# Kernel tuning notes

Hardware: AMD Instinct MI355X
Metric: run time of the kernel (lower is better)

## Reference

```python
import jax, jax.numpy as jnp
import numpy as np

B, NR, NP, E, F, EIN, H, OUT = 2, 16384, 65536, 262144, 128, 4, 16, 4
EPS = 1e-6

def _mlp(x, W1, b1, W2, b2):
    return jax.nn.swish(x @ W1 + b1) @ W2 + b2

def _cond_norm(x, tau, C1, c1, C2, c2):
    # conditioned LayerNorm: scale/shift computed from tau by a shallow MLP
    h = jax.nn.swish(tau @ C1 + c1)               # [B, H]
    scale, shift = jnp.split(h @ C2 + c2, 2, -1)  # [B, F] each
    mu = jnp.mean(x, -1, keepdims=True)
    var = jnp.var(x, -1, keepdims=True)
    xn = (x - mu) * jax.lax.rsqrt(var + EPS)
    return xn * (1.0 + scale[:, None, :]) + shift[:, None, :]

def _segment_mean(feat, recv, num_segments):
    seg = lambda f, r: jax.ops.segment_sum(f, r, num_segments=num_segments)
    s = jax.vmap(seg)(feat, recv)
    cnt = jax.vmap(seg)(jnp.ones(recv.shape, feat.dtype), recv)
    return s / jnp.maximum(cnt, 1.0)[..., None]

def setup_inputs():
    key = jax.random.key(0)
    ks = iter(jax.random.split(key, 48))
    dense = lambda i, o: jax.random.normal(next(ks), (i, o), jnp.float32) / np.sqrt(i)
    inp = {}
    inp['rnode_features'] = jax.random.normal(next(ks), (B, NR, F), jnp.float32)
    inp['pnode_features'] = jax.random.normal(next(ks), (B, NP, F), jnp.float32)
    inp['edge_features'] = jax.random.normal(next(ks), (B, E, EIN), jnp.float32)
    inp['tau'] = jax.random.uniform(next(ks), (B, 1), jnp.float32)
    # edge embedding MLP + cond norm
    inp['We1'], inp['We2'] = dense(EIN, F), dense(F, F)
    inp['be1'], inp['be2'] = jnp.zeros((F,)), jnp.zeros((F,))
    inp['Ce1'], inp['Ce2'] = dense(1, H), dense(H, 2 * F)
    inp['ce1'], inp['ce2'] = jnp.zeros((H,)), jnp.zeros((2 * F,))
    # edge update MLP + cond norm
    inp['Wu1'], inp['Wu2'] = dense(3 * F, F), dense(F, F)
    inp['bu1'], inp['bu2'] = jnp.zeros((F,)), jnp.zeros((F,))
    inp['Cu1'], inp['Cu2'] = dense(1, H), dense(H, 2 * F)
    inp['cu1'], inp['cu2'] = jnp.zeros((H,)), jnp.zeros((2 * F,))
    # pnode update MLP + cond norm
    inp['Wp1'], inp['Wp2'] = dense(2 * F, F), dense(F, F)
    inp['bp1'], inp['bp2'] = jnp.zeros((F,)), jnp.zeros((F,))
    inp['Cp1'], inp['Cp2'] = dense(1, H), dense(H, 2 * F)
    inp['cp1'], inp['cp2'] = jnp.zeros((H,)), jnp.zeros((2 * F,))
    # rnode update MLP + cond norm
    inp['Wr1'], inp['Wr2'] = dense(F, F), dense(F, F)
    inp['br1'], inp['br2'] = jnp.zeros((F,)), jnp.zeros((F,))
    inp['Cr1'], inp['Cr2'] = dense(1, H), dense(H, 2 * F)
    inp['cr1'], inp['cr2'] = jnp.zeros((H,)), jnp.zeros((2 * F,))
    # pnode output MLP (no norm)
    inp['Wo1'], inp['Wo2'] = dense(F, F), dense(F, OUT)
    inp['bo1'], inp['bo2'] = jnp.zeros((F,)), jnp.zeros((OUT,))
    inp['senders'] = jax.random.randint(next(ks), (B, E), 0, NR, jnp.int32)
    inp['receivers'] = jax.random.randint(next(ks), (B, E), 0, NP, jnp.int32)
    return inp

def reference(rnode_features, pnode_features, edge_features, tau,
              We1, be1, We2, be2, Ce1, ce1, Ce2, ce2,
              Wu1, bu1, Wu2, bu2, Cu1, cu1, Cu2, cu2,
              Wp1, bp1, Wp2, bp2, Cp1, cp1, Cp2, cp2,
              Wr1, br1, Wr2, br2, Cr1, cr1, Cr2, cr2,
              Wo1, bo1, Wo2, bo2, senders, receivers):
    # 1) embed raw r2p edge features to latent size (embed_edges=True)
    e = _cond_norm(_mlp(edge_features, We1, be1, We2, be2), tau, Ce1, ce1, Ce2, ce2)
    # 2) one message-passing step: edge update from gathered sender/receiver feats
    sf = jnp.take_along_axis(rnode_features, senders[..., None], axis=1)    # [B,E,F]
    rf = jnp.take_along_axis(pnode_features, receivers[..., None], axis=1)  # [B,E,F]
    e = e + _cond_norm(_mlp(jnp.concatenate([e, sf, rf], -1), Wu1, bu1, Wu2, bu2),
                       tau, Cu1, cu1, Cu2, cu2)
    # 3) pnode update with segment_mean aggregation, residual
    agg = _segment_mean(e, receivers, NP)                                   # [B,NP,F]
    p = pnode_features + _cond_norm(
        _mlp(jnp.concatenate([pnode_features, agg], -1), Wp1, bp1, Wp2, bp2),
        tau, Cp1, cp1, Cp2, cp2)
    # 4) rnode update (no incoming edges; structurally present but unused by output)
    r = rnode_features + _cond_norm(_mlp(rnode_features, Wr1, br1, Wr2, br2),
                                    tau, Cr1, cr1, Cr2, cr2)
    del r
    # 5) output MLP on pnodes (node_output_size=dict(pnodes=num_outputs))
    return _mlp(p, Wo1, bo1, Wo2, bo2)
```

## Files before the change

kernel.cpp:

```cpp
#include <hip/hip_runtime.h>

constexpr int cB  = 2;
constexpr int cNR = 16384;
constexpr int cNP = 65536;
constexpr int cE  = 262144;
constexpr int cF  = 128;
constexpr int SP  = 136;

typedef unsigned short u16;
using f32x4 = __attribute__((ext_vector_type(4))) float;
using s8v   = __attribute__((ext_vector_type(8))) short;

constexpr size_t WS_CNT = ((size_t)cB * cNP * cF) / 2;
constexpr size_t WS_SS  = WS_CNT + (size_t)cB * cNP;
constexpr size_t WS_WB  = WS_SS + 3 * cB * 256;

constexpr int G8_We2 = 0, G8_Wu1 = 16, G8_Wu2 = 64, G8_Wp1 = 80, G8_Wp2 = 112, G8_Wo1 = 128;
constexpr int G8_TOT = 144;
constexpr int SWZ_N = G8_TOT * 128 + 256;
constexpr size_t WS_RB = WS_WB + (size_t)SWZ_N * 4;

__device__ __forceinline__ float bf2f(u16 u) {
  union { unsigned int i; float f; } v; v.i = ((unsigned int)u) << 16; return v.f;
}
__device__ __forceinline__ u16 f2bf(float f) {
  union { float f; unsigned int i; } v; v.f = f;
  unsigned int x = v.i;
  return (u16)((x + 0x7fffu + ((x >> 16) & 1u)) >> 16);
}
__device__ __forceinline__ u16 f2bf_fast(float f) {
  return (u16)((__float_as_uint(f) + 0x8000u) >> 16);
}
__device__ __forceinline__ unsigned pack2(float a, float b) {
  return __builtin_amdgcn_perm(__float_as_uint(b) + 0x8000u,
                               __float_as_uint(a) + 0x8000u, 0x07060302u);
}
__device__ __forceinline__ float swishf(float x) {
  return x * __builtin_amdgcn_rcpf(1.0f + __expf(-x));
}

template <int CTRL>
__device__ __forceinline__ float dpp_add(float x) {
  int xi = __float_as_int(x);
  int r = __builtin_amdgcn_update_dpp(xi, xi, CTRL, 0xf, 0xf, false);
  return x + __int_as_float(r);
}
__device__ __forceinline__ float dpp_xor1(float x) {
  int xi = __float_as_int(x);
  int r = __builtin_amdgcn_update_dpp(xi, xi, 0xB1, 0xf, 0xf, false);
  return __int_as_float(r);
}

__device__ __forceinline__ void atomic_pk_bf16(u16* addr, float lo, float hi) {
  unsigned data = pack2(lo, hi);
  unsigned long long a = (unsigned long long)addr;
  asm volatile("global_atomic_pk_add_bf16 %0, %1, off" :: "v"(a), "v"(data) : "memory");
}

__device__ __forceinline__ void kloop128s(const u16* act, const u16* __restrict__ wbg,
                                          f32x4 (&acc)[4][2], int cw, int l16, int quad) {
  s8v bf[4][2];
#pragma unroll
  for (int k0 = 0; k0 < 4; ++k0)
#pragma unroll
    for (int ci = 0; ci < 2; ++ci)
      bf[k0][ci] = *(const s8v*)(wbg + ((size_t)(k0 * 4 + quad) * 128 + cw + ci * 16 + l16) * 8);
#pragma unroll
  for (int k0 = 0; k0 < 4; ++k0) {
    s8v af[4];
#pragma unroll
    for (int ri = 0; ri < 4; ++ri)
      af[ri] = *(const s8v*)(act + (size_t)(ri * 16 + l16) * SP + k0 * 32 + quad * 8);
#pragma unroll
    for (int ri = 0; ri < 4; ++ri)
#pragma unroll
      for (int ci = 0; ci < 2; ++ci)
        acc[ri][ci] = __builtin_amdgcn_mfma_f32_16x16x32_bf16(af[ri], bf[k0][ci], acc[ri][ci], 0, 0, 0);
  }
}

__device__ __forceinline__ void init_acc_s(f32x4 (&acc)[4][2], const float* __restrict__ bias,
                                           int cw, int l16) {
#pragma unroll
  for (int ci = 0; ci < 2; ++ci) {
    float bv = bias[cw + ci * 16 + l16];
#pragma unroll
    for (int ri = 0; ri < 4; ++ri) acc[ri][ci] = (f32x4){bv, bv, bv, bv};
  }
}

__device__ __forceinline__ void cond_norm_s(f32x4 (&acc)[4][2], float* red, float* musig,
                                            const float* __restrict__ ssp,
                                            int cw, int l16, int quad, int wv, int t) {
  __syncthreads();
#pragma unroll
  for (int ri = 0; ri < 4; ++ri)
#pragma unroll
    for (int reg = 0; reg < 4; ++reg) {
      float v0 = acc[ri][0][reg], v1 = acc[ri][1][reg];
      float s = v0 + v1;
      float q = v0 * v0 + v1 * v1;
      s = dpp_add<0x128>(s); q = dpp_add<0x128>(q);
      s = dpp_add<0x124>(s); q = dpp_add<0x124>(q);
      s = dpp_add<0x122>(s); q = dpp_add<0x122>(q);
      s = dpp_add<0x121>(s); q = dpp_add<0x121>(q);
      if (l16 == 0) {
        int row = ri * 16 + quad * 4 + reg;
        red[row * 8 + wv * 2]     = s;
        red[row * 8 + wv * 2 + 1] = q;
      }
    }
  __syncthreads();
  if (t < 64) {
    float sum = red[t * 8 + 0] + red[t * 8 + 2] + red[t * 8 + 4] + red[t * 8 + 6];
    float sq  = red[t * 8 + 1] + red[t * 8 + 3] + red[t * 8 + 5] + red[t * 8 + 7];
    float mu  = sum * (1.0f / 128.0f);
    float var = fmaxf(sq * (1.0f / 128.0f) - mu * mu, 0.0f);
    musig[t * 2]     = mu;
    musig[t * 2 + 1] = __builtin_amdgcn_rsqf(var + 1e-6f);
  }
  __syncthreads();
  float scl[2], shf[2];
#pragma unroll
  for (int ci = 0; ci < 2; ++ci) {
    int col = cw + ci * 16 + l16;
    scl[ci] = 1.0f + ssp[col];
    shf[ci] = ssp[128 + col];
  }
#pragma unroll
  for (int ri = 0; ri < 4; ++ri)
#pragma unroll
    for (int reg = 0; reg < 4; ++reg) {
      int row = ri * 16 + quad * 4 + reg;
      float mu = musig[row * 2], is = musig[row * 2 + 1];
#pragma unroll
      for (int ci = 0; ci < 2; ++ci)
        acc[ri][ci][reg] = (acc[ri][ci][reg] - mu) * is * scl[ci] + shf[ci];
    }
}

template <bool DOSWISH>
__device__ __forceinline__ void store_s(u16* buf, const f32x4 (&acc)[4][2],
                                        int cw, int l16, int quad) {
#pragma unroll
  for (int ri = 0; ri < 4; ++ri)
#pragma unroll
    for (int reg = 0; reg < 4; ++reg) {
      int row = ri * 16 + quad * 4 + reg;
#pragma unroll
      for (int ci = 0; ci < 2; ++ci) {
        float v = acc[ri][ci][reg];
        if (DOSWISH) v = swishf(v);
        buf[(size_t)row * SP + cw + ci * 16 + l16] = f2bf_fast(v);
      }
    }
}

__global__ void zero_kernel(float4* __restrict__ p, int n4) {
  int i = blockIdx.x * 256 + threadIdx.x;
  if (i < n4) p[i] = make_float4(0.f, 0.f, 0.f, 0.f);
}

__global__ void cvtn_kernel(const float* __restrict__ src, u16* __restrict__ dst, int n2) {
  int i = blockIdx.x * 256 + threadIdx.x;
  if (i >= n2) return;
  float2 v = ((const float2*)src)[i];
  ((unsigned*)dst)[i] = pack2(v.x, v.y);
}

struct SwzSrc { const float* p[6]; };

__global__ void swz_kernel(SwzSrc s, const float* __restrict__ Wo2, u16* __restrict__ wb) {
  int t = blockIdx.x * 256 + threadIdx.x;
  if (t >= SWZ_N) return;
  if (t >= G8_TOT * 128) {
    int idx2 = t - G8_TOT * 128;
    int k8 = idx2 >> 4, n = idx2 & 15;
    u16 v[8];
#pragma unroll
    for (int j = 0; j < 8; ++j)
      v[j] = (n < 4) ? f2bf(Wo2[(size_t)(k8 * 8 + j) * 4 + n]) : (u16)0;
    ((uint4*)wb)[G8_TOT * 128 + k8 * 16 + n] = *(uint4*)v;
    return;
  }
  int n = t & 127, g8 = t >> 7;
  int seg, base;
  if (g8 < G8_Wu1)      { seg = 0; base = G8_We2; }
  else if (g8 < G8_Wu2) { seg = 1; base = G8_Wu1; }
  else if (g8 < G8_Wp1) { seg = 2; base = G8_Wu2; }
  else if (g8 < G8_Wp2) { seg = 3; base = G8_Wp1; }
  else if (g8 < G8_Wo1) { seg = 4; base = G8_Wp2; }
  else                  { seg = 5; base = G8_Wo1; }
  const float* W = s.p[seg];
  int k8l = g8 - base;
  u16 v[8];
#pragma unroll
  for (int j = 0; j < 8; ++j) v[j] = f2bf(W[(size_t)(k8l * 8 + j) * 128 + n]);
  ((uint4*)wb)[g8 * 128 + n] = *(uint4*)v;
}

__global__ void cond_kernel(const float* __restrict__ tau,
                            const float* __restrict__ Ce1, const float* __restrict__ ce1,
                            const float* __restrict__ Ce2, const float* __restrict__ ce2,
                            const float* __restrict__ Cu1, const float* __restrict__ cu1,
                            const float* __restrict__ Cu2, const float* __restrict__ cu2,
                            const float* __restrict__ Cp1, const float* __restrict__ cp1,
                            const float* __restrict__ Cp2, const float* __restrict__ cp2,
                            float* __restrict__ ss) {
  int set = blockIdx.x, b = blockIdx.y, j = threadIdx.x;
  const float *C1, *c1, *C2, *c2;
  if (set == 0)      { C1 = Ce1; c1 = ce1; C2 = Ce2; c2 = ce2; }
  else if (set == 1) { C1 = Cu1; c1 = cu1; C2 = Cu2; c2 = cu2; }
  else               { C1 = Cp1; c1 = cp1; C2 = Cp2; c2 = cp2; }
  float tf = tau[b];
  float a = c2[j];
  for (int k = 0; k < 16; ++k) {
    float h = swishf(tf * C1[k] + c1[k]);
    a = fmaf(h, C2[k * 256 + j], a);
  }
  ss[(size_t)set * cB * 256 + (size_t)b * 256 + j] = a;
}

struct EWb { const float *We1, *be1, *be2, *bu1, *bu2; };

struct __align__(16) EdgeSmem {
  u16 bufE[64 * SP];
  u16 bufX[64 * SP];
  float ef4[256];
  float red[512];
  float musig[128];
  int sidx[64], ridx[64];
};

__global__ __launch_bounds__(256, 4) void edge_mfma(
    const u16* __restrict__ rnb, const float* __restrict__ pnode,
    const float* __restrict__ efeat, const int* __restrict__ senders,
    const int* __restrict__ receivers, EWb w, const u16* __restrict__ wb,
    const float* __restrict__ ss, u16* __restrict__ aggb, float* __restrict__ cnt) {
  __shared__ EdgeSmem sm;
  const int t = threadIdx.x, wv = t >> 6, lane = t & 63, l16 = lane & 15, quad = lane >> 4;
  const int cw = wv * 32;
  const int b  = blockIdx.y;
  const int e0 = blockIdx.x * 64;

  if (t < 64) {
    sm.sidx[t] = min(max(senders[(size_t)b * cE + e0 + t], 0), cNR - 1);
    sm.ridx[t] = min(max(receivers[(size_t)b * cE + e0 + t], 0), cNP - 1);
  } else if (t >= 128) {
    ((float2*)sm.ef4)[t - 128] = ((const float2*)(efeat + ((size_t)b * cE + e0) * 4))[t - 128];
  }
  __syncthreads();

  unsigned rfp[16];
#pragma unroll
  for (int rr = 0; rr < 16; ++rr) {
    int row = wv * 16 + rr;
    unsigned sv = *(const unsigned*)(rnb + ((size_t)b * cNR + sm.sidx[row]) * cF + lane * 2);
    float2 rv = *(const float2*)(pnode + ((size_t)b * cNP + sm.ridx[row]) * cF + lane * 2);
    *(unsigned*)(sm.bufX + (size_t)row * SP + lane * 2) = sv;
    rfp[rr] = pack2(rv.x, rv.y);
  }

  {
    int col = t & 127, half = t >> 7;
    float w0 = w.We1[col], w1 = w.We1[128 + col], w2 = w.We1[256 + col], w3 = w.We1[384 + col];
    float bb = w.be1[col];
    for (int r = 0; r < 32; ++r) {
      int row = half * 32 + r;
      float a = fmaf(sm.ef4[row * 4 + 3], w3, fmaf(sm.ef4[row * 4 + 2], w2,
                fmaf(sm.ef4[row * 4 + 1], w1, fmaf(sm.ef4[row * 4 + 0], w0, bb))));
      sm.bufE[(size_t)row * SP + col] = f2bf_fast(swishf(a));
    }
  }
  __syncthreads();

  f32x4 acc[4][2];

  init_acc_s(acc, w.be2, cw, l16);
  kloop128s(sm.bufE, wb + (size_t)G8_We2 * 1024, acc, cw, l16, quad);
  cond_norm_s(acc, sm.red, sm.musig, ss + (size_t)b * 256, cw, l16, quad, wv, t);
  store_s<false>(sm.bufE, acc, cw, l16, quad);
  __syncthreads();

  f32x4 accU[4][2];
  init_acc_s(accU, w.bu1, cw, l16);
  kloop128s(sm.bufE, wb + (size_t)G8_Wu1 * 1024, accU, cw, l16, quad);
  kloop128s(sm.bufX, wb + (size_t)(G8_Wu1 + 16) * 1024, accU, cw, l16, quad);
  __syncthreads();

#pragma unroll
  for (int rr = 0; rr < 16; ++rr)
    *(unsigned*)(sm.bufX + (size_t)(wv * 16 + rr) * SP + lane * 2) = rfp[rr];
  __syncthreads();

  kloop128s(sm.bufX, wb + (size_t)(G8_Wu1 + 32) * 1024, accU, cw, l16, quad);
  __syncthreads();
  store_s<true>(sm.bufX, accU, cw, l16, quad);
  __syncthreads();

  init_acc_s(acc, w.bu2, cw, l16);
  kloop128s(sm.bufX, wb + (size_t)G8_Wu2 * 1024, acc, cw, l16, quad);
  cond_norm_s(acc, sm.red, sm.musig, ss + (size_t)(cB + b) * 256, cw, l16, quad, wv, t);

#pragma unroll
  for (int ri = 0; ri < 4; ++ri)
#pragma unroll
    for (int reg = 0; reg < 4; ++reg) {
      int row = ri * 16 + quad * 4 + reg;
      size_t rbase = ((size_t)b * cNP + sm.ridx[row]) * cF;
#pragma unroll
      for (int ci = 0; ci < 2; ++ci) {
        int col = cw + ci * 16 + l16;
        float v = acc[ri][ci][reg] + bf2f(sm.bufE[(size_t)row * SP + col]);
        float vo = dpp_xor1(v);
        if (!(lane & 1)) atomic_pk_bf16(aggb + rbase + col, v, vo);
      }
    }
  if (t < 64) atomicAdd(cnt + (size_t)b * cNP + sm.ridx[t], 1.0f);
}

struct PWb { const float *bp1, *bp2, *bo1, *bo2; };

struct __align__(16) PnodeSmem {
  u16 bufP[64 * SP];
  u16 bufX[64 * SP];
  float red[512];
  float musig[128];
  float cinv[64];
};

__global__ __launch_bounds__(256, 4) void pnode_mfma(
    const float* __restrict__ pnode, PWb w, const u16* __restrict__ wb,
    const float* __restrict__ ss, const u16* __restrict__ aggb,
    const float* __restrict__ cnt, float* __restrict__ out) {
  __shared__ PnodeSmem sm;
  const int t = threadIdx.x, wv = t >> 6, lane = t & 63, l16 = lane & 15, quad = lane >> 4;
  const int cw = wv * 32;
  const int b  = blockIdx.y;
  const int n0 = blockIdx.x * 64;

  if (t < 64) sm.cinv[t] = __builtin_amdgcn_rcpf(fmaxf(cnt[(size_t)b * cNP + n0 + t], 1.0f));
  __syncthreads();

#pragma unroll
  for (int rr = 0; rr < 16; ++rr) {
    int row = wv * 16 + rr;
    float2 pv = *(const float2*)(pnode + ((size_t)b * cNP + n0 + row) * cF + lane * 2);
    unsigned avu = *(const unsigned*)(aggb + (((size_t)b * cNP + n0 + row) * cF + lane * 2));
    float ci_ = sm.cinv[row];
    float a0 = bf2f((u16)(avu & 0xffffu)) * ci_;
    float a1 = bf2f((u16)(avu >> 16)) * ci_;
    *(unsigned*)(sm.bufP + (size_t)row * SP + lane * 2) = pack2(pv.x, pv.y);
    *(unsigned*)(sm.bufX + (size_t)row * SP + lane * 2) = pack2(a0, a1);
  }
  __syncthreads();

  f32x4 acc[4][2];

  init_acc_s(acc, w.bp1, cw, l16);
  kloop128s(sm.bufP, wb + (size_t)G8_Wp1 * 1024, acc, cw, l16, quad);
  kloop128s(sm.bufX, wb + (size_t)(G8_Wp1 + 16) * 1024, acc, cw, l16, quad);
  __syncthreads();
  store_s<true>(sm.bufX, acc, cw, l16, quad);
  __syncthreads();

  init_acc_s(acc, w.bp2, cw, l16);
  kloop128s(sm.bufX, wb + (size_t)G8_Wp2 * 1024, acc, cw, l16, quad);
  cond_norm_s(acc, sm.red, sm.musig, ss + (size_t)(2 * cB + b) * 256, cw, l16, quad, wv, t);
#pragma unroll
  for (int ri = 0; ri < 4; ++ri)
#pragma unroll
    for (int reg = 0; reg < 4; ++reg) {
      int row = ri * 16 + quad * 4 + reg;
#pragma unroll
      for (int ci = 0; ci < 2; ++ci)
        acc[ri][ci][reg] += bf2f(sm.bufP[(size_t)row * SP + cw + ci * 16 + l16]);
    }
  __syncthreads();
  store_s<false>(sm.bufP, acc, cw, l16, quad);
  __syncthreads();

  init_acc_s(acc, w.bo1, cw, l16);
  kloop128s(sm.bufP, wb + (size_t)G8_Wo1 * 1024, acc, cw, l16, quad);
  store_s<true>(sm.bufX, acc, cw, l16, quad);
  __syncthreads();

  {
    const u16* wo2 = wb + (size_t)G8_TOT * 1024;
    float bv = (l16 < 4) ? w.bo2[l16] : 0.0f;
    f32x4 a1 = {bv, bv, bv, bv};
#pragma unroll
    for (int k0 = 0; k0 < 4; ++k0) {
      s8v af = *(const s8v*)(sm.bufX + (size_t)(wv * 16 + l16) * SP + k0 * 32 + quad * 8);
      s8v bf = *(const s8v*)(wo2 + ((size_t)(k0 * 4 + quad) * 16 + l16) * 8);
      a1 = __builtin_amdgcn_mfma_f32_16x16x32_bf16(af, bf, a1, 0, 0, 0);
    }
    if (l16 < 4) {
      size_t obase = (size_t)b * cNP + n0 + wv * 16 + quad * 4;
#pragma unroll
      for (int reg = 0; reg < 4; ++reg)
        out[(obase + reg) * 4 + l16] = a1[reg];
    }
  }
}

extern "C" void kernel_launch(void* const* d_in, const int* in_sizes, int n_in,
                              void* d_out, int out_size, void* d_ws, size_t ws_size,
                              hipStream_t stream) {
  const float* rnode = (const float*)d_in[0];
  const float* pnode = (const float*)d_in[1];
  const float* efeat = (const float*)d_in[2];
  const float* tau   = (const float*)d_in[3];
  const int* senders   = (const int*)d_in[40];
  const int* receivers = (const int*)d_in[41];
  float* ws = (float*)d_ws;
  u16* aggb = (u16*)d_ws;
  u16* wb   = (u16*)(ws + WS_WB);
  u16* rnb  = (u16*)(ws + WS_RB);

  SwzSrc sw;
  sw.p[0] = (const float*)d_in[5];
  sw.p[1] = (const float*)d_in[12];
  sw.p[2] = (const float*)d_in[13];
  sw.p[3] = (const float*)d_in[20];
  sw.p[4] = (const float*)d_in[21];
  sw.p[5] = (const float*)d_in[36];
  swz_kernel<<<(SWZ_N + 255) / 256, 256, 0, stream>>>(sw, (const float*)d_in[37], wb);

  const int nrn2 = (int)((size_t)cB * cNR * cF / 2);
  cvtn_kernel<<<(nrn2 + 255) / 256, 256, 0, stream>>>(rnode, rnb, nrn2);

  cond_kernel<<<dim3(3, cB), 256, 0, stream>>>(
      tau,
      (const float*)d_in[8],  (const float*)d_in[10],
      (const float*)d_in[9],  (const float*)d_in[11],
      (const float*)d_in[16], (const float*)d_in[18],
      (const float*)d_in[17], (const float*)d_in[19],
      (const float*)d_in[24], (const float*)d_in[26],
      (const float*)d_in[25], (const float*)d_in[27],
      ws + WS_SS);

  EWb ew = { (const float*)d_in[4], (const float*)d_in[6], (const float*)d_in[7],
             (const float*)d_in[14], (const float*)d_in[15] };
  PWb pw = { (const float*)d_in[22], (const float*)d_in[23], (const float*)d_in[38],
             (const float*)d_in[39] };

  const int n4 = (int)(WS_SS / 4);
  zero_kernel<<<(n4 + 255) / 256, 256, 0, stream>>>((float4*)ws, n4);

  edge_mfma<<<dim3(cE / 64, cB), 256, 0, stream>>>(
      rnb, pnode, efeat, senders, receivers, ew, wb,
      ws + WS_SS, aggb, ws + WS_CNT);

  pnode_mfma<<<dim3(cNP / 64, cB), 256, 0, stream>>>(
      pnode, pw, wb, ws + WS_SS, aggb, ws + WS_CNT,
      (float*)d_out);
}
```

Before: 565.4 us.

## Process two edge tiles per block and prefetch second tile's gathers

Each edge block now handles 128 edges as two 64-row tiles. The sender and receiver feature gathers for the second tile are issued while the first tile is still computing, which is meant to hide gather latency. Indices are stored as u16. __syncthreads is replaced with a raw s_waitcnt lgkmcnt(0)+s_barrier that does not wait on outstanding global loads. The extra prefetch registers (rfv float2[16], sfp1[16]) raise register pressure under launch_bounds(256,4), and the grid has half as many blocks.

Result: slower. 728.8 us (+28.9%).

```diff
diff --git a/kernel.cpp b/kernel.cpp
--- a/kernel.cpp
+++ b/kernel.cpp
@@ -39,6 +39,10 @@
   return x * __builtin_amdgcn_rcpf(1.0f + __expf(-x));
 }
 
+__device__ __forceinline__ void lds_barrier() {
+  asm volatile("s_waitcnt lgkmcnt(0)\n\ts_barrier" ::: "memory");
+}
+
 template <int CTRL>
 __device__ __forceinline__ float dpp_add(float x) {
   int xi = __float_as_int(x);
@@ -92,7 +96,7 @@
 __device__ __forceinline__ void cond_norm_s(f32x4 (&acc)[4][2], float* red, float* musig,
                                             const float* __restrict__ ssp,
                                             int cw, int l16, int quad, int wv, int t) {
-  __syncthreads();
+  lds_barrier();
 #pragma unroll
   for (int ri = 0; ri < 4; ++ri)
 #pragma unroll
@@ -110,7 +114,7 @@
         red[row * 8 + wv * 2 + 1] = q;
       }
     }
-  __syncthreads();
+  lds_barrier();
   if (t < 64) {
     float sum = red[t * 8 + 0] + red[t * 8 + 2] + red[t * 8 + 4] + red[t * 8 + 6];
     float sq  = red[t * 8 + 1] + red[t * 8 + 3] + red[t * 8 + 5] + red[t * 8 + 7];
@@ -119,7 +123,7 @@
     musig[t * 2]     = mu;
     musig[t * 2 + 1] = __builtin_amdgcn_rsqf(var + 1e-6f);
   }
-  __syncthreads();
+  lds_barrier();
   float scl[2], shf[2];
 #pragma unroll
   for (int ci = 0; ci < 2; ++ci) {
@@ -226,11 +230,80 @@
 struct __align__(16) EdgeSmem {
   u16 bufE[64 * SP];
   u16 bufX[64 * SP];
-  float ef4[256];
+  float ef4[512];
   float red[512];
   float musig[128];
-  int sidx[64], ridx[64];
+  u16 sidx[128], ridx[128];
 };
+
+__device__ __forceinline__ void embed_l1(EdgeSmem& sm, const EWb& w, int io, int t) {
+  int col = t & 127, half = t >> 7;
+  float w0 = w.We1[col], w1 = w.We1[128 + col], w2 = w.We1[256 + col], w3 = w.We1[384 + col];
+  float bb = w.be1[col];
+  for (int r = 0; r < 32; ++r) {
+    int row = half * 32 + r;
+    const float* e4 = sm.ef4 + (io + row) * 4;
+    float a = fmaf(e4[3], w3, fmaf(e4[2], w2, fmaf(e4[1], w1, fmaf(e4[0], w0, bb))));
+    sm.bufE[(size_t)row * SP + col] = f2bf_fast(swishf(a));
+  }
+}
+
+template <bool PRE>
+__device__ __forceinline__ void edge_tile(
+    EdgeSmem& sm, const EWb& w, const u16* __restrict__ wb,
+    const float* __restrict__ ss, u16* __restrict__ aggb,
+    const float* __restrict__ pnode, float2 (&rfv)[16], int io, int b,
+    int cw, int l16, int quad, int wv, int t, int lane) {
+  f32x4 acc[4][2];
+
+  init_acc_s(acc, w.be2, cw, l16);
+  kloop128s(sm.bufE, wb + (size_t)G8_We2 * 1024, acc, cw, l16, quad);
+  cond_norm_s(acc, sm.red, sm.musig, ss + (size_t)b * 256, cw, l16, quad, wv, t);
+  store_s<false>(sm.bufE, acc, cw, l16, quad);
+  lds_barrier();
+
+  f32x4 accU[4][2];
+  init_acc_s(accU, w.bu1, cw, l16);
+  kloop128s(sm.bufE, wb + (size_t)G8_Wu1 * 1024, accU, cw, l16, quad);
+  kloop128s(sm.bufX, wb + (size_t)(G8_Wu1 + 16) * 1024, accU, cw, l16, quad);
+  lds_barrier();
+
+#pragma unroll
+  for (int rr = 0; rr < 16; ++rr)
+    *(unsigned*)(sm.bufX + (size_t)(wv * 16 + rr) * SP + lane * 2) = pack2(rfv[rr].x, rfv[rr].y);
+  if (PRE) {
+#pragma unroll
+    for (int rr = 0; rr < 16; ++rr) {
+      int row = wv * 16 + rr;
+      rfv[rr] = *(const float2*)(pnode + ((size_t)b * cNP + sm.ridx[64 + row]) * cF + lane * 2);
+    }
+  }
+  lds_barrier();
+
+  kloop128s(sm.bufX, wb + (size_t)(G8_Wu1 + 32) * 1024, accU, cw, l16, quad);
+  lds_barrier();
+  store_s<true>(sm.bufX, accU, cw, l16, quad);
+  lds_barrier();
+
+  init_acc_s(acc, w.bu2, cw, l16);
+  kloop128s(sm.bufX, wb + (size_t)G8_Wu2 * 1024, acc, cw, l16, quad);
+  cond_norm_s(acc, sm.red, sm.musig, ss + (size_t)(cB + b) * 256, cw, l16, quad, wv, t);
+
+#pragma unroll
+  for (int ri = 0; ri < 4; ++ri)
+#pragma unroll
+    for (int reg = 0; reg < 4; ++reg) {
+      int row = ri * 16 + quad * 4 + reg;
+      size_t rbase = ((size_t)b * cNP + sm.ridx[io + row]) * cF;
+#pragma unroll
+      for (int ci = 0; ci < 2; ++ci) {
+        int col = cw + ci * 16 + l16;
+        float v = acc[ri][ci][reg] + bf2f(sm.bufE[(size_t)row * SP + col]);
+        float vo = dpp_xor1(v);
+        if (!(lane & 1)) atomic_pk_bf16(aggb + rbase + col, v, vo);
+      }
+    }
+}
 
 __global__ __launch_bounds__(256, 4) void edge_mfma(
     const u16* __restrict__ rnb, const float* __restrict__ pnode,
@@ -241,82 +314,40 @@
   const int t = threadIdx.x, wv = t >> 6, lane = t & 63, l16 = lane & 15, quad = lane >> 4;
   const int cw = wv * 32;
   const int b  = blockIdx.y;
-  const int e0 = blockIdx.x * 64;
-
-  if (t < 64) {
-    sm.sidx[t] = min(max(senders[(size_t)b * cE + e0 + t], 0), cNR - 1);
-    sm.ridx[t] = min(max(receivers[(size_t)b * cE + e0 + t], 0), cNP - 1);
-  } else if (t >= 128) {
-    ((float2*)sm.ef4)[t - 128] = ((const float2*)(efeat + ((size_t)b * cE + e0) * 4))[t - 128];
-  }
-  __syncthreads();
-
-  unsigned rfp[16];
+  const int e0 = blockIdx.x * 128;
+
+  if (t < 128) {
+    sm.sidx[t] = (u16)min(max(senders[(size_t)b * cE + e0 + t], 0), cNR - 1);
+    sm.ridx[t] = (u16)min(max(receivers[(size_t)b * cE + e0 + t], 0), cNP - 1);
+  }
+  ((float2*)sm.ef4)[t] = ((const float2*)(efeat + ((size_t)b * cE + e0) * 4))[t];
+  lds_barrier();
+
+  float2 rfv[16];
+  unsigned sfp1[16];
 #pragma unroll
   for (int rr = 0; rr < 16; ++rr) {
     int row = wv * 16 + rr;
     unsigned sv = *(const unsigned*)(rnb + ((size_t)b * cNR + sm.sidx[row]) * cF + lane * 2);
-    float2 rv = *(const float2*)(pnode + ((size_t)b * cNP + sm.ridx[row]) * cF + lane * 2);
+    rfv[rr] = *(const float2*)(pnode + ((size_t)b * cNP + sm.ridx[row]) * cF + lane * 2);
+    sfp1[rr] = *(const unsigned*)(rnb + ((size_t)b * cNR + sm.sidx[64 + row]) * cF + lane * 2);
     *(unsigned*)(sm.bufX + (size_t)row * SP + lane * 2) = sv;
-    rfp[rr] = pack2(rv.x, rv.y);
-  }
-
-  {
-    int col = t & 127, half = t >> 7;
-    float w0 = w.We1[col], w1 = w.We1[128 + col], w2 = w.We1[256 + col], w3 = w.We1[384 + col];
-    float bb = w.be1[col];
-    for (int r = 0; r < 32; ++r) {
-      int row = half * 32 + r;
-      float a = fmaf(sm.ef4[row * 4 + 3], w3, fmaf(sm.ef4[row * 4 + 2], w2,
-                fmaf(sm.ef4[row * 4 + 1], w1, fmaf(sm.ef4[row * 4 + 0], w0, bb))));
-      sm.bufE[(size_t)row * SP + col] = f2bf_fast(swishf(a));
-    }
-  }
-  __syncthreads();
-
-  f32x4 acc[4][2];
-
-  init_acc_s(acc, w.be2, cw, l16);
-  kloop128s(sm.bufE, wb + (size_t)G8_We2 * 1024, acc, cw, l16, quad);
-  cond_norm_s(acc, sm.red, sm.musig, ss + (size_t)b * 256, cw, l16, quad, wv, t);
-  store_s<false>(sm.bufE, acc, cw, l16, quad);
-  __syncthreads();
-
-  f32x4 accU[4][2];
-  init_acc_s(accU, w.bu1, cw, l16);
-  kloop128s(sm.bufE, wb + (size_t)G8_Wu1 * 1024, accU, cw, l16, quad);
-  kloop128s(sm.bufX, wb + (size_t)(G8_Wu1 + 16) * 1024, accU, cw, l16, quad);
-  __syncthreads();
+  }
+  embed_l1(sm, w, 0, t);
+  lds_barrier();
+
+  edge_tile<true>(sm, w, wb, ss, aggb, pnode, rfv, 0, b, cw, l16, quad, wv, t, lane);
+
+  if (t < 128) atomicAdd(cnt + (size_t)b * cNP + sm.ridx[t], 1.0f);
+  lds_barrier();
 
 #pragma unroll
   for (int rr = 0; rr < 16; ++rr)
-    *(unsigned*)(sm.bufX + (size_t)(wv * 16 + rr) * SP + lane * 2) = rfp[rr];
-  __syncthreads();
-
-  kloop128s(sm.bufX, wb + (size_t)(G8_Wu1 + 32) * 1024, accU, cw, l16, quad);
-  __syncthreads();
-  store_s<true>(sm.bufX, accU, cw, l16, quad);
-  __syncthreads();
-
-  init_acc_s(acc, w.bu2, cw, l16);
-  kloop128s(sm.bufX, wb + (size_t)G8_Wu2 * 1024, acc, cw, l16, quad);
-  cond_norm_s(acc, sm.red, sm.musig, ss + (size_t)(cB + b) * 256, cw, l16, quad, wv, t);
-
-#pragma unroll
-  for (int ri = 0; ri < 4; ++ri)
-#pragma unroll
-    for (int reg = 0; reg < 4; ++reg) {
-      int row = ri * 16 + quad * 4 + reg;
-      size_t rbase = ((size_t)b * cNP + sm.ridx[row]) * cF;
-#pragma unroll
-      for (int ci = 0; ci < 2; ++ci) {
-        int col = cw + ci * 16 + l16;
-        float v = acc[ri][ci][reg] + bf2f(sm.bufE[(size_t)row * SP + col]);
-        float vo = dpp_xor1(v);
-        if (!(lane & 1)) atomic_pk_bf16(aggb + rbase + col, v, vo);
-      }
-    }
-  if (t < 64) atomicAdd(cnt + (size_t)b * cNP + sm.ridx[t], 1.0f);
+    *(unsigned*)(sm.bufX + (size_t)(wv * 16 + rr) * SP + lane * 2) = sfp1[rr];
+  embed_l1(sm, w, 64, t);
+  lds_barrier();
+
+  edge_tile<false>(sm, w, wb, ss, aggb, pnode, rfv, 64, b, cw, l16, quad, wv, t, lane);
 }
 
 struct PWb { const float *bp1, *bp2, *bo1, *bo2; };
@@ -340,7 +371,7 @@
   const int n0 = blockIdx.x * 64;
 
   if (t < 64) sm.cinv[t] = __builtin_amdgcn_rcpf(fmaxf(cnt[(size_t)b * cNP + n0 + t], 1.0f));
-  __syncthreads();
+  lds_barrier();
 
 #pragma unroll
   for (int rr = 0; rr < 16; ++rr) {
@@ -353,16 +384,16 @@
     *(unsigned*)(sm.bufP + (size_t)row * SP + lane * 2) = pack2(pv.x, pv.y);
     *(unsigned*)(sm.bufX + (size_t)row * SP + lane * 2) = pack2(a0, a1);
   }
-  __syncthreads();
+  lds_barrier();
 
   f32x4 acc[4][2];
 
   init_acc_s(acc, w.bp1, cw, l16);
   kloop128s(sm.bufP, wb + (size_t)G8_Wp1 * 1024, acc, cw, l16, quad);
   kloop128s(sm.bufX, wb + (size_t)(G8_Wp1 + 16) * 1024, acc, cw, l16, quad);
-  __syncthreads();
+  lds_barrier();
   store_s<true>(sm.bufX, acc, cw, l16, quad);
-  __syncthreads();
+  lds_barrier();
 
   init_acc_s(acc, w.bp2, cw, l16);
   kloop128s(sm.bufX, wb + (size_t)G8_Wp2 * 1024, acc, cw, l16, quad);
@@ -376,14 +407,14 @@
       for (int ci = 0; ci < 2; ++ci)
         acc[ri][ci][reg] += bf2f(sm.bufP[(size_t)row * SP + cw + ci * 16 + l16]);
     }
-  __syncthreads();
+  lds_barrier();
   store_s<false>(sm.bufP, acc, cw, l16, quad);
-  __syncthreads();
+  lds_barrier();
 
   init_acc_s(acc, w.bo1, cw, l16);
   kloop128s(sm.bufP, wb + (size_t)G8_Wo1 * 1024, acc, cw, l16, quad);
   store_s<true>(sm.bufX, acc, cw, l16, quad);
-  __syncthreads();
+  lds_barrier();
 
   {
     const u16* wo2 = wb + (size_t)G8_TOT * 1024;
@@ -448,7 +479,7 @@
   const int n4 = (int)(WS_SS / 4);
   zero_kernel<<<(n4 + 255) / 256, 256, 0, stream>>>((float4*)ws, n4);
 
-  edge_mfma<<<dim3(cE / 64, cB), 256, 0, stream>>>(
+  edge_mfma<<<dim3(cE / 128, cB), 256, 0, stream>>>(
       rnb, pnode, efeat, senders, receivers, ew, wb,
       ws + WS_SS, aggb, ws + WS_CNT);
 
```
